# Performance work log

Measured on AMD Instinct MI355X. Metric: run time of the kernel, lower is better.

Reference implementation:

```python
import jax, jax.numpy as jnp
import numpy as np
from jax import lax

B, T, D, H = 64, 512, 256, 256


def lstm_scan(x_seq, Wih, Whh, bih, bhh):
    """Run an LSTMCell over time. x_seq: [B, T, D] -> hidden states [B, T, H].
    Gate order i, f, g, o (torch LSTMCell convention)."""
    Bv, Tv, _ = x_seq.shape
    Hv = Whh.shape[1]
    # Precompute input projection once: [B, T, 4H]
    x_proj = jnp.einsum('btd,gd->btg', x_seq, Wih) + bih + bhh

    def step(carry, xp):
        h, c = carry
        gates = xp + h @ Whh.T  # [B, 4H]
        i, f, g, o = jnp.split(gates, 4, axis=-1)
        c = jax.nn.sigmoid(f) * c + jax.nn.sigmoid(i) * jnp.tanh(g)
        h = jax.nn.sigmoid(o) * jnp.tanh(c)
        return (h, c), h

    init = (jnp.zeros((Bv, Hv), x_seq.dtype), jnp.zeros((Bv, Hv), x_seq.dtype))
    _, hs = lax.scan(step, init, jnp.swapaxes(x_proj, 0, 1))  # [T, B, H]
    return jnp.swapaxes(hs, 0, 1)


def bilstm(x, input_length, Wih_f, Whh_f, bih_f, bhh_f, Wih_b, Whh_b, bih_b, bhh_b):
    Bv, L, _ = x.shape
    t = jnp.arange(L)
    lens = input_length.astype(jnp.int32)
    # Inversed input exactly as _get_inversed_input: for t < len -> x[len-1-t],
    # for t >= len -> x[L-1-(t-len)] (unused tail, faithful to original).
    inv_idx = L - 1 - ((L - lens[:, None] + t[None, :]) % L)  # [B, L]
    xn = jnp.take_along_axis(x, inv_idx[:, :, None], axis=1)

    fwd_h = lstm_scan(x, Wih_f, Whh_f, bih_f, bhh_f)   # [B, L, H]
    bwd_h = lstm_scan(xn, Wih_b, Whh_b, bih_b, bhh_b)  # [B, L, H]

    # Re-reverse the backward states over valid region; zero-pad beyond length.
    mask = t[None, :] < lens[:, None]                   # [B, L]
    bwd_idx = jnp.clip(lens[:, None] - 1 - t[None, :], 0, L - 1)
    bwd_g = jnp.take_along_axis(bwd_h, bwd_idx[:, :, None], axis=1)
    out = jnp.concatenate([fwd_h, bwd_g], axis=-1)      # [B, L, 2H]
    return jnp.where(mask[:, :, None], out, jnp.zeros((), out.dtype))


def setup_inputs() -> dict:
    key = jax.random.key(0)
    ks = jax.random.split(key, 10)
    s = 0.05
    return {
        'x': jax.random.normal(ks[0], (B, T, D), jnp.float32),
        'input_length': jax.random.randint(ks[1], (B,), 1, T + 1, jnp.int32),
        'Wih_f': jax.random.normal(ks[2], (4 * H, D), jnp.float32) * s,
        'Whh_f': jax.random.normal(ks[3], (4 * H, H), jnp.float32) * s,
        'bih_f': jax.random.normal(ks[4], (4 * H,), jnp.float32) * s,
        'bhh_f': jax.random.normal(ks[5], (4 * H,), jnp.float32) * s,
        'Wih_b': jax.random.normal(ks[6], (4 * H, D), jnp.float32) * s,
        'Whh_b': jax.random.normal(ks[7], (4 * H, H), jnp.float32) * s,
        'bih_b': jax.random.normal(ks[8], (4 * H,), jnp.float32) * s,
        'bhh_b': jax.random.normal(ks[9], (4 * H,), jnp.float32) * s,
    }


def reference(x, input_length, Wih_f, Whh_f, bih_f, bhh_f, Wih_b, Whh_b, bih_b, bhh_b):
    return bilstm(x, input_length, Wih_f, Whh_f, bih_f, bhh_f, Wih_b, Whh_b, bih_b, bhh_b)
```

## Files before the change

kernel.cpp:

```cpp
#include <hip/hip_runtime.h>
#include <cstdio>


typedef unsigned short ushort_t;
typedef __attribute__((ext_vector_type(8))) short short8;
typedef __attribute__((ext_vector_type(4))) float f32x4;
typedef __attribute__((ext_vector_type(4))) int i32x4;

__device__ __forceinline__ ushort_t f2bf(float f) {
    union { float f; unsigned u; } v; v.f = f;
    unsigned r = v.u + 0x7fffu + ((v.u >> 16) & 1u);
    return (ushort_t)(r >> 16);
}
__device__ __forceinline__ float bf2f(ushort_t h) {
    union { unsigned u; float f; } v; v.u = ((unsigned)h) << 16;
    return v.f;
}

__device__ __forceinline__ float fexp2(float x) {
#if __has_builtin(__builtin_amdgcn_exp2f)
    return __builtin_amdgcn_exp2f(x);
#else
    return exp2f(x);
#endif
}
__device__ __forceinline__ float frcp(float x) {
#if __has_builtin(__builtin_amdgcn_rcpf)
    return __builtin_amdgcn_rcpf(x);
#else
    return 1.0f / x;
#endif
}
__device__ __forceinline__ float fsig(float x) {
    return frcp(1.0f + fexp2(-1.44269504089f * x));
}
__device__ __forceinline__ float ftanh(float x) {
    float e = fexp2(2.88539008178f * x);
    return 1.0f - 2.0f * frcp(e + 1.0f);
}

__device__ __forceinline__ void lds_barrier() {
    asm volatile("s_waitcnt lgkmcnt(0)\n\ts_barrier" ::: "memory");
}

__global__ __launch_bounds__(256) void k_f2bf(const float* __restrict__ in,
                                              ushort_t* __restrict__ out, int n) {
    int i = (blockIdx.x * 256 + threadIdx.x) * 4;
    if (i + 3 < n) {
        float4 v = *(const float4*)&in[i];
        ushort4 o;
        o.x = f2bf(v.x); o.y = f2bf(v.y); o.z = f2bf(v.z); o.w = f2bf(v.w);
        *(ushort4*)&out[i] = o;
    }
}

__global__ __launch_bounds__(256) void k_wih(const float* __restrict__ wihf,
                                             const float* __restrict__ wihb,
                                             ushort_t* __restrict__ dst) {
    int d = blockIdx.y;
    int n = blockIdx.x * 4 + (threadIdx.x >> 6);
    int l = threadIdx.x & 63;
    const float* src = (d ? wihb : wihf) + (size_t)n * 256;
    float4 v = *(const float4*)&src[l * 4];
    int np = (n & 255) * 4 + (n >> 8);
    ushort4 o;
    o.x = f2bf(v.x); o.y = f2bf(v.y); o.z = f2bf(v.z); o.w = f2bf(v.w);
    *(ushort4*)&dst[((size_t)d * 1024 + np) * 256 + l * 4] = o;
}

__global__ __launch_bounds__(256) void k_bias(const float* __restrict__ bihf,
                                              const float* __restrict__ bhhf,
                                              const float* __restrict__ bihb,
                                              const float* __restrict__ bhhb,
                                              float* __restrict__ bv) {
    int i = blockIdx.x * 256 + threadIdx.x;
    int d = i >> 10, n = i & 1023;
    float s = d ? (bihb[n] + bhhb[n]) : (bihf[n] + bhhf[n]);
    bv[d * 1024 + (n & 255) * 4 + (n >> 8)] = s;
}

__global__ __launch_bounds__(256) void k_quant(const float* __restrict__ whhf,
                                               const float* __restrict__ whhb,
                                               int* __restrict__ wmf,
                                               float* __restrict__ fscale4) {
    int rowg = blockIdx.x * 4 + (threadIdx.x >> 6);
    int l = threadIdx.x & 63;
    int d = rowg >> 10;
    int row = rowg & 1023;
    const float* W = (d ? whhb : whhf) + (size_t)row * 256;
    float4 v = *(const float4*)&W[l * 4];
    float m = fmaxf(fmaxf(fabsf(v.x), fabsf(v.y)), fmaxf(fabsf(v.z), fabsf(v.w)));
    #pragma unroll
    for (int off = 32; off > 0; off >>= 1) m = fmaxf(m, __shfl_xor(m, off));
    float inv = (m > 0.0f) ? (127.0f / m) : 0.0f;
    int q0 = __float2int_rn(v.x * inv);
    int q1 = __float2int_rn(v.y * inv);
    int q2 = __float2int_rn(v.z * inv);
    int q3 = __float2int_rn(v.w * inv);
    q0 = min(127, max(-127, q0)); q1 = min(127, max(-127, q1));
    q2 = min(127, max(-127, q2)); q3 = min(127, max(-127, q3));
    int packed = (q0 & 255) | ((q1 & 255) << 8) | ((q2 & 255) << 16) | ((q3 & 255) << 24);
    int j = row & 255, gate = row >> 8;
    int row_p = j * 4 + gate;
    int Mt = row_p >> 4, rl = row_p & 15;
    int Kt = l >> 4, lg = (l >> 2) & 3, dw = l & 3;
    wmf[d * 65536 + ((Mt * 4 + Kt) * 64 + lg * 16 + rl) * 4 + dw] = packed;
    if (l == 0) fscale4[d * 1024 + row_p] = m / (127.0f * 127.0f);
}

#define LDSOFF(r, kc) ((r) * 32 + ((((kc) + ((r) >> 1)) & 3) * 8))

__global__ __launch_bounds__(256) void k_gemm(const ushort_t* __restrict__ A,
                                              const ushort_t* __restrict__ Bw,
                                              const float* __restrict__ biasv,
                                              ushort_t* __restrict__ Xp) {
    const int dir = blockIdx.z;
    const ushort_t* Bmat = Bw + dir * 262144;
    const float* bv = biasv + dir * 1024;
    ushort_t* C = Xp + (size_t)dir * 33554432;
    const int tn = blockIdx.x;
    const int tm = blockIdx.y;
    const int tid = threadIdx.x;
    const int w = tid >> 6, l = tid & 63;
    const int wm = w & 1, wn = w >> 1;

    __shared__ ushort_t As[128 * 32];
    __shared__ ushort_t Bs[128 * 32];

    f32x4 acc[4][4];
    #pragma unroll
    for (int i = 0; i < 4; i++)
        #pragma unroll
        for (int jj = 0; jj < 4; jj++) acc[i][jj] = (f32x4){0.f, 0.f, 0.f, 0.f};

    const int r0 = tid >> 2, c0 = tid & 3;
    const int r1 = (tid + 256) >> 2, c1 = tid & 3;

    for (int kb = 0; kb < 8; kb++) {
        __syncthreads();
        {
            short8 a0 = *(const short8*)&A[((size_t)(tm * 128 + r0)) * 256 + kb * 32 + c0 * 8];
            short8 a1 = *(const short8*)&A[((size_t)(tm * 128 + r1)) * 256 + kb * 32 + c1 * 8];
            short8 b0 = *(const short8*)&Bmat[((size_t)(tn * 128 + r0)) * 256 + kb * 32 + c0 * 8];
            short8 b1 = *(const short8*)&Bmat[((size_t)(tn * 128 + r1)) * 256 + kb * 32 + c1 * 8];
            *(short8*)&As[LDSOFF(r0, c0)] = a0;
            *(short8*)&As[LDSOFF(r1, c1)] = a1;
            *(short8*)&Bs[LDSOFF(r0, c0)] = b0;
            *(short8*)&Bs[LDSOFF(r1, c1)] = b1;
        }
        __syncthreads();
        short8 af[4], bfr[4];
        const int q = l >> 4;
        #pragma unroll
        for (int mt = 0; mt < 4; mt++) {
            int rr = wm * 64 + mt * 16 + (l & 15);
            af[mt] = *(const short8*)&As[LDSOFF(rr, q)];
        }
        #pragma unroll
        for (int nt = 0; nt < 4; nt++) {
            int rr = wn * 64 + nt * 16 + (l & 15);
            bfr[nt] = *(const short8*)&Bs[LDSOFF(rr, q)];
        }
        #pragma unroll
        for (int mt = 0; mt < 4; mt++)
            #pragma unroll
            for (int nt = 0; nt < 4; nt++)
                acc[mt][nt] = __builtin_amdgcn_mfma_f32_16x16x32_bf16(
                    af[mt], bfr[nt], acc[mt][nt], 0, 0, 0);
    }
    #pragma unroll
    for (int nt = 0; nt < 4; nt++) {
        int n = tn * 128 + wn * 64 + nt * 16 + (l & 15);
        float bn = bv[n];
        #pragma unroll
        for (int mt = 0; mt < 4; mt++) {
            #pragma unroll
            for (int rr = 0; rr < 4; rr++) {
                int m = tm * 128 + wm * 64 + mt * 16 + (l >> 4) * 4 + rr;
                C[(size_t)m * 1024 + n] = f2bf(acc[mt][nt][rr] + bn);
            }
        }
    }
}

__device__ __forceinline__ int time_idx(int s, int len, int d) {
    int sc = (s < len - 1) ? s : (len - 1);
    return (d == 0) ? sc : (len - 1 - sc);
}

__global__ __launch_bounds__(512, 2) void k_rec(const ushort_t* __restrict__ xproj,
                                                const int* __restrict__ wmf,
                                                const float* __restrict__ fscale4,
                                                const int* __restrict__ lens,
                                                float* __restrict__ out) {
    const int b = blockIdx.x, d = blockIdx.y;
    const int tid = threadIdx.x;
    const int w = tid >> 6, l = tid & 63;
    int len = lens[b];
    if (len < 1) len = 1;
    if (len > 512) len = 512;
    const ushort_t* xp = xproj + ((size_t)d * 64 + b) * 524288;

    const int rg = l >> 4;
    const int til = l & 7;
    const bool act = (l & 15) < 8;
    const int j = (w * 8 + til) * 4 + rg;

    i32x4 wf[8][4];
    const int* wb = wmf + d * 65536;
    #pragma unroll
    for (int i = 0; i < 8; i++)
        #pragma unroll
        for (int kt = 0; kt < 4; kt++)
            wf[i][kt] = *(const i32x4*)&wb[(((w * 8 + i) * 4 + kt) * 64 + l) * 4];
    #pragma unroll
    for (int i = 0; i < 8; i++)
        #pragma unroll
        for (int kt = 0; kt < 4; kt++)
            asm volatile("" : "+v"(wf[i][kt]));

    float4 fr = *(const float4*)&fscale4[d * 1024 + 4 * j];

    __shared__ char h8[2][256] __attribute__((aligned(16)));
    if (tid < 64) ((int*)h8)[tid] = 0;

    {
        float4 z = {0.f, 0.f, 0.f, 0.f};
        int total4 = (512 - len) * 64;
        for (int i = tid; i < total4; i += 512) {
            int t = len + (i >> 6);
            int c4 = i & 63;
            *(float4*)&out[((size_t)b * 512 + t) * 512 + d * 256 + c4 * 4] = z;
        }
    }
    __syncthreads();

    float c_state = 0.0f;
    uint2 xv0 = *(const uint2*)&xp[(size_t)time_idx(0, len, d) * 1024 + 4 * j];
    uint2 xv1 = *(const uint2*)&xp[(size_t)time_idx(1, len, d) * 1024 + 4 * j];
    const i32x4 z4 = {0, 0, 0, 0};

    for (int s = 0; s < len; s++) {
        uint2 xc = xv0;
        xv0 = xv1;
        uint2 xn = *(const uint2*)&xp[(size_t)time_idx(s + 2, len, d) * 1024 + 4 * j];

        const char* hb = h8[s & 1];
        i32x4 h0 = *(const i32x4*)(hb + rg * 16);
        i32x4 h1 = *(const i32x4*)(hb + 64 + rg * 16);
        i32x4 h2 = *(const i32x4*)(hb + 128 + rg * 16);
        i32x4 h3 = *(const i32x4*)(hb + 192 + rg * 16);

        i32x4 acc[8];
        #pragma unroll
        for (int i = 0; i < 8; i++) {
            i32x4 a = __builtin_amdgcn_mfma_i32_16x16x64_i8(wf[i][0], h0, z4, 0, 0, 0);
            a = __builtin_amdgcn_mfma_i32_16x16x64_i8(wf[i][1], h1, a, 0, 0, 0);
            a = __builtin_amdgcn_mfma_i32_16x16x64_i8(wf[i][2], h2, a, 0, 0, 0);
            acc[i] = __builtin_amdgcn_mfma_i32_16x16x64_i8(wf[i][3], h3, a, 0, 0, 0);
        }

        if (act) {
            i32x4 q0 = (til & 1) ? acc[1] : acc[0];
            i32x4 q1 = (til & 1) ? acc[3] : acc[2];
            i32x4 q2 = (til & 1) ? acc[5] : acc[4];
            i32x4 q3 = (til & 1) ? acc[7] : acc[6];
            i32x4 r0 = (til & 2) ? q1 : q0;
            i32x4 r1 = (til & 2) ? q3 : q2;
            i32x4 u  = (til & 4) ? r1 : r0;
            float pi = bf2f((ushort_t)(xc.x & 0xffffu)) + fr.x * (float)u.x;
            float pf = bf2f((ushort_t)(xc.x >> 16))     + fr.y * (float)u.y;
            float pg = bf2f((ushort_t)(xc.y & 0xffffu)) + fr.z * (float)u.z;
            float po = bf2f((ushort_t)(xc.y >> 16))     + fr.w * (float)u.w;
            float ig = fsig(pi), fg = fsig(pf), gg = ftanh(pg), og = fsig(po);
            c_state = fg * c_state + ig * gg;
            float h = og * ftanh(c_state);
            int t = time_idx(s, len, d);
            out[((size_t)b * 512 + t) * 512 + d * 256 + j] = h;
            int q = __float2int_rn(h * 127.0f);
            q = min(127, max(-127, q));
            h8[1 - (s & 1)][j] = (char)q;
        }
        xv1 = xn;
        lds_barrier();
    }
}

extern "C" void kernel_launch(void* const* d_in, const int* in_sizes, int n_in,
                              void* d_out, int out_size, void* d_ws, size_t ws_size,
                              hipStream_t stream) {
    (void)in_sizes; (void)n_in; (void)out_size;
    const float* x    = (const float*)d_in[0];
    const int*   lens = (const int*)d_in[1];
    const float* wihf = (const float*)d_in[2];
    const float* whhf = (const float*)d_in[3];
    const float* bihf = (const float*)d_in[4];
    const float* bhhf = (const float*)d_in[5];
    const float* wihb = (const float*)d_in[6];
    const float* whhb = (const float*)d_in[7];
    const float* bihb = (const float*)d_in[8];
    const float* bhhb = (const float*)d_in[9];
    float* out = (float*)d_out;

    char* ws = (char*)d_ws;
    ushort_t* xbf    = (ushort_t*)(ws + 0);
    ushort_t* wihbf  = (ushort_t*)(ws + 16777216);
    float*    biasv  = (float*)(ws + 17825792);
    int*      wmf    = (int*)(ws + 17833984);
    float*    fscale4= (float*)(ws + 18358272);
    ushort_t* xproj  = (ushort_t*)(ws + 18366464);
    const size_t REQ = 18366464 + 134217728ull;
    if (ws_size < REQ) {
        fprintf(stderr, "kernel_launch: ws too small: %zu < %zu\n", ws_size, REQ);
    }

    k_f2bf<<<8192, 256, 0, stream>>>(x, xbf, 8388608);
    k_wih<<<dim3(256, 2), 256, 0, stream>>>(wihf, wihb, wihbf);
    k_bias<<<8, 256, 0, stream>>>(bihf, bhhf, bihb, bhhb, biasv);
    k_quant<<<512, 256, 0, stream>>>(whhf, whhb, wmf, fscale4);
    k_gemm<<<dim3(8, 256, 2), 256, 0, stream>>>(xbf, wihbf, biasv, xproj);
    k_rec<<<dim3(64, 2), 512, 0, stream>>>(xproj, wmf, fscale4, lens, out);
}
```

Baseline: 562.2 us.

## Halve recurrent block to 4 waves with 16 tiles each, all lanes active

```diff
diff --git a/kernel.cpp b/kernel.cpp
--- a/kernel.cpp
+++ b/kernel.cpp
@@ -188,7 +188,7 @@
     return (d == 0) ? sc : (len - 1 - sc);
 }
 
-__global__ __launch_bounds__(512, 2) void k_rec(const ushort_t* __restrict__ xproj,
+__global__ __launch_bounds__(256, 1) void k_rec(const ushort_t* __restrict__ xproj,
                                                 const int* __restrict__ wmf,
                                                 const float* __restrict__ fscale4,
                                                 const int* __restrict__ lens,
@@ -202,22 +202,17 @@
     const ushort_t* xp = xproj + ((size_t)d * 64 + b) * 524288;
 
     const int rg = l >> 4;
-    const int til = l & 7;
-    const bool act = (l & 15) < 8;
-    const int j = (w * 8 + til) * 4 + rg;
-
-    i32x4 wf[8][4];
+    const int j = (w * 16 + (l & 15)) * 4 + rg;
+
+    i32x4 wf[16][4];
     const int* wb = wmf + d * 65536;
     #pragma unroll
-    for (int i = 0; i < 8; i++)
-        #pragma unroll
-        for (int kt = 0; kt < 4; kt++)
-            wf[i][kt] = *(const i32x4*)&wb[(((w * 8 + i) * 4 + kt) * 64 + l) * 4];
-    #pragma unroll
-    for (int i = 0; i < 8; i++)
-        #pragma unroll
-        for (int kt = 0; kt < 4; kt++)
-            asm volatile("" : "+v"(wf[i][kt]));
+    for (int til = 0; til < 16; til++)
+        #pragma unroll
+        for (int kt = 0; kt < 4; kt++) {
+            wf[til][kt] = *(const i32x4*)&wb[(((w * 16 + til) * 4 + kt) * 64 + l) * 4];
+            asm volatile("" : "+a"(wf[til][kt]));
+        }
 
     float4 fr = *(const float4*)&fscale4[d * 1024 + 4 * j];
 
@@ -227,7 +222,7 @@
     {
         float4 z = {0.f, 0.f, 0.f, 0.f};
         int total4 = (512 - len) * 64;
-        for (int i = tid; i < total4; i += 512) {
+        for (int i = tid; i < total4; i += 256) {
             int t = len + (i >> 6);
             int c4 = i & 63;
             *(float4*)&out[((size_t)b * 512 + t) * 512 + d * 256 + c4 * 4] = z;
@@ -238,50 +233,64 @@
     float c_state = 0.0f;
     uint2 xv0 = *(const uint2*)&xp[(size_t)time_idx(0, len, d) * 1024 + 4 * j];
     uint2 xv1 = *(const uint2*)&xp[(size_t)time_idx(1, len, d) * 1024 + 4 * j];
+    uint2 xv2 = *(const uint2*)&xp[(size_t)time_idx(2, len, d) * 1024 + 4 * j];
     const i32x4 z4 = {0, 0, 0, 0};
 
     for (int s = 0; s < len; s++) {
-        uint2 xc = xv0;
-        xv0 = xv1;
-        uint2 xn = *(const uint2*)&xp[(size_t)time_idx(s + 2, len, d) * 1024 + 4 * j];
-
         const char* hb = h8[s & 1];
         i32x4 h0 = *(const i32x4*)(hb + rg * 16);
         i32x4 h1 = *(const i32x4*)(hb + 64 + rg * 16);
         i32x4 h2 = *(const i32x4*)(hb + 128 + rg * 16);
         i32x4 h3 = *(const i32x4*)(hb + 192 + rg * 16);
 
-        i32x4 acc[8];
-        #pragma unroll
-        for (int i = 0; i < 8; i++) {
-            i32x4 a = __builtin_amdgcn_mfma_i32_16x16x64_i8(wf[i][0], h0, z4, 0, 0, 0);
-            a = __builtin_amdgcn_mfma_i32_16x16x64_i8(wf[i][1], h1, a, 0, 0, 0);
-            a = __builtin_amdgcn_mfma_i32_16x16x64_i8(wf[i][2], h2, a, 0, 0, 0);
-            acc[i] = __builtin_amdgcn_mfma_i32_16x16x64_i8(wf[i][3], h3, a, 0, 0, 0);
-        }
-
-        if (act) {
-            i32x4 q0 = (til & 1) ? acc[1] : acc[0];
-            i32x4 q1 = (til & 1) ? acc[3] : acc[2];
-            i32x4 q2 = (til & 1) ? acc[5] : acc[4];
-            i32x4 q3 = (til & 1) ? acc[7] : acc[6];
-            i32x4 r0 = (til & 2) ? q1 : q0;
-            i32x4 r1 = (til & 2) ? q3 : q2;
-            i32x4 u  = (til & 4) ? r1 : r0;
-            float pi = bf2f((ushort_t)(xc.x & 0xffffu)) + fr.x * (float)u.x;
-            float pf = bf2f((ushort_t)(xc.x >> 16))     + fr.y * (float)u.y;
-            float pg = bf2f((ushort_t)(xc.y & 0xffffu)) + fr.z * (float)u.z;
-            float po = bf2f((ushort_t)(xc.y >> 16))     + fr.w * (float)u.w;
-            float ig = fsig(pi), fg = fsig(pf), gg = ftanh(pg), og = fsig(po);
-            c_state = fg * c_state + ig * gg;
-            float h = og * ftanh(c_state);
-            int t = time_idx(s, len, d);
-            out[((size_t)b * 512 + t) * 512 + d * 256 + j] = h;
-            int q = __float2int_rn(h * 127.0f);
-            q = min(127, max(-127, q));
-            h8[1 - (s & 1)][j] = (char)q;
-        }
-        xv1 = xn;
+        uint2 xc = xv0;
+        xv0 = xv1;
+        xv1 = xv2;
+        xv2 = *(const uint2*)&xp[(size_t)time_idx(s + 3, len, d) * 1024 + 4 * j];
+
+        i32x4 acc[16];
+        #pragma unroll
+        for (int til = 0; til < 16; til++)
+            acc[til] = __builtin_amdgcn_mfma_i32_16x16x64_i8(wf[til][0], h0, z4, 0, 0, 0);
+        #pragma unroll
+        for (int til = 0; til < 16; til++)
+            acc[til] = __builtin_amdgcn_mfma_i32_16x16x64_i8(wf[til][1], h1, acc[til], 0, 0, 0);
+        #pragma unroll
+        for (int til = 0; til < 16; til++)
+            acc[til] = __builtin_amdgcn_mfma_i32_16x16x64_i8(wf[til][2], h2, acc[til], 0, 0, 0);
+        #pragma unroll
+        for (int til = 0; til < 16; til++)
+            acc[til] = __builtin_amdgcn_mfma_i32_16x16x64_i8(wf[til][3], h3, acc[til], 0, 0, 0);
+
+        i32x4 a0 = (l & 1) ? acc[1] : acc[0];
+        i32x4 a1 = (l & 1) ? acc[3] : acc[2];
+        i32x4 a2 = (l & 1) ? acc[5] : acc[4];
+        i32x4 a3 = (l & 1) ? acc[7] : acc[6];
+        i32x4 a4 = (l & 1) ? acc[9] : acc[8];
+        i32x4 a5 = (l & 1) ? acc[11] : acc[10];
+        i32x4 a6 = (l & 1) ? acc[13] : acc[12];
+        i32x4 a7 = (l & 1) ? acc[15] : acc[14];
+        i32x4 b0 = (l & 2) ? a1 : a0;
+        i32x4 b1 = (l & 2) ? a3 : a2;
+        i32x4 b2 = (l & 2) ? a5 : a4;
+        i32x4 b3 = (l & 2) ? a7 : a6;
+        i32x4 c0 = (l & 4) ? b1 : b0;
+        i32x4 c1 = (l & 4) ? b3 : b2;
+        i32x4 u  = (l & 8) ? c1 : c0;
+
+        float pi = bf2f((ushort_t)(xc.x & 0xffffu)) + fr.x * (float)u.x;
+        float pf = bf2f((ushort_t)(xc.x >> 16))     + fr.y * (float)u.y;
+        float pg = bf2f((ushort_t)(xc.y & 0xffffu)) + fr.z * (float)u.z;
+        float po = bf2f((ushort_t)(xc.y >> 16))     + fr.w * (float)u.w;
+        float ig = fsig(pi), fg = fsig(pf), gg = ftanh(pg), og = fsig(po);
+        c_state = fg * c_state + ig * gg;
+        float h = og * ftanh(c_state);
+        int q = __float2int_rn(h * 127.0f);
+        q = min(127, max(-127, q));
+        h8[1 - (s & 1)][j] = (char)q;
+        int t = time_idx(s, len, d);
+        out[((size_t)b * 512 + t) * 512 + d * 256 + j] = h;
+
         lds_barrier();
     }
 }
@@ -319,5 +328,5 @@
     k_bias<<<8, 256, 0, stream>>>(bihf, bhhf, bihb, bhhb, biasv);
     k_quant<<<512, 256, 0, stream>>>(whhf, whhb, wmf, fscale4);
     k_gemm<<<dim3(8, 256, 2), 256, 0, stream>>>(xbf, wihbf, biasv, xproj);
-    k_rec<<<dim3(64, 2), 512, 0, stream>>>(xproj, wmf, fscale4, lens, out);
-}
+    k_rec<<<dim3(64, 2), 256, 0, stream>>>(xproj, wmf, fscale4, lens, out);
+}
```

Result: slower. 619.0 us (+10.1%).
